# Kernel optimization log

Hardware: AMD Instinct MI355X
Metric: run time of the kernel (lower is better)

## Reference

```python
import jax, jax.numpy as jnp
import numpy as np

B, G, C = 16384, 7, 30  # batch, 7x7 grid, 2*5 box params + 20 classes


def setup_inputs() -> dict:
    key = jax.random.key(0)
    k1, k2 = jax.random.split(key)
    pred = jax.random.uniform(k1, (B, G, G, C), dtype=jnp.float32)
    labels = jax.random.uniform(k2, (B, G, G, C), dtype=jnp.float32)
    # channel 0 of labels is the object-presence indicator (==1 where a gt box exists)
    labels = labels.at[..., 0].set((labels[..., 0] > 0.7).astype(jnp.float32))
    return {"pred": pred, "labels": labels}


def _corners(box):
    # box channels: [conf, x, y, w, h]
    x, y, w, h = box[..., 1], box[..., 2], box[..., 3], box[..., 4]
    return x - 0.5 * w, x + 0.5 * w, y - 0.5 * h, y + 0.5 * h  # left,right,top,bottom


def _iou(b1, b2):
    l1, r1, t1, bt1 = _corners(b1)
    l2, r2, t2, bt2 = _corners(b2)
    in_h = jnp.minimum(bt1, bt2) - jnp.maximum(t1, t2)
    in_w = jnp.minimum(r1, r2) - jnp.maximum(l1, l2)
    inter = jnp.where((in_h < 0) | (in_w < 0), 0.0, in_h * in_w)
    area1 = (bt1 - t1) * (r1 - l1)
    area2 = (bt2 - t2) * (r2 - l2)
    return inter / (area1 + area2 - inter)


def reference(pred, labels):
    mask = labels[..., 0]                     # [B,7,7] object indicator (0/1)
    box1 = pred[..., 0:5]
    box2 = pred[..., 5:10]
    gt = labels[..., 0:5]
    iou1 = _iou(box1, gt)
    iou2 = _iou(box2, gt)
    best = iou1 >= iou2                       # responsible box per cell
    sel = jnp.where(best[..., None], box1, box2)
    iou_max = jnp.where(best, iou1, iou2)
    iou_min = jnp.where(best, iou2, iou1)
    center = 5.0 * ((sel[..., 1] - gt[..., 1]) ** 2 + (sel[..., 2] - gt[..., 2]) ** 2)
    wh = 5.0 * ((jnp.sqrt(sel[..., 3]) - jnp.sqrt(gt[..., 3])) ** 2
                + (jnp.sqrt(sel[..., 4]) - jnp.sqrt(gt[..., 4])) ** 2)
    cls = jnp.sum((pred[..., 10:] - labels[..., 10:]) ** 2, axis=-1)

    def msum(x):
        return jnp.sum(x * mask)

    # [center, wh, obj_conf, noobj_conf, classification]
    return jnp.stack([msum(center), msum(wh), msum(iou_max), msum(iou_min), msum(cls)])
```

## Files before the change

### kernel.cpp

```cpp
#include <hip/hip_runtime.h>
#include <stdint.h>

#define NCH   30
#define TPB   256
#define CPB   256
#define WORDS (CPB * NCH)
#define TOTW  (2 * WORDS)
#define NF4   (TOTW / 4)
#define ITERS (NF4 / TPB)

__device__ __forceinline__ float iou_f(float x1, float y1, float w1, float h1,
                                       float x2, float y2, float w2, float h2) {
    float l1 = x1 - 0.5f * w1, r1 = x1 + 0.5f * w1;
    float t1 = y1 - 0.5f * h1, b1 = y1 + 0.5f * h1;
    float l2 = x2 - 0.5f * w2, r2 = x2 + 0.5f * w2;
    float t2 = y2 - 0.5f * h2, b2 = y2 + 0.5f * h2;
    float in_h = fminf(b1, b2) - fmaxf(t1, t2);
    float in_w = fminf(r1, r2) - fmaxf(l1, l2);
    float inter = (in_h < 0.f || in_w < 0.f) ? 0.f : in_h * in_w;
    float a1 = (b1 - t1) * (r1 - l1);
    float a2 = (b2 - t2) * (r2 - l2);
    return inter / (a1 + a2 - inter);
}

__global__ __launch_bounds__(TPB) void yolo_partial(const float* __restrict__ pred,
                                                    const float* __restrict__ lab,
                                                    float* __restrict__ partial,
                                                    int n_cells) {
    __shared__ float s[TOTW];
    __shared__ float red[5][TPB / 64];

    const int tid = threadIdx.x;
    const int base_cell = blockIdx.x * CPB;
    const size_t base_word = (size_t)base_cell * NCH;
    const int cells_here = min(CPB, n_cells - base_cell);

    if (cells_here == CPB) {
#pragma unroll
        for (int it = 0; it < ITERS; ++it) {
            const int idx = it * TPB + tid;
            const float* src = (idx < WORDS / 4)
                ? (pred + base_word + (size_t)idx * 4)
                : (lab  + base_word + (size_t)(idx - WORDS / 4) * 4);
            __builtin_amdgcn_global_load_lds(
                (const __attribute__((address_space(1))) uint32_t*)src,
                (__attribute__((address_space(3))) uint32_t*)(s + idx * 4),
                16, 0, 0);
        }
    } else {
        const int nw = cells_here * NCH;
        for (int w = tid; w < nw; w += TPB) {
            s[w]         = pred[base_word + w];
            s[WORDS + w] = lab [base_word + w];
        }
    }
    __syncthreads();

    float v0 = 0.f, v1 = 0.f, v2 = 0.f, v3 = 0.f, v4 = 0.f;

    if (tid < cells_here) {
        const float* pp = s + tid * NCH;
        const float* lp = s + WORDS + tid * NCH;

        const float2 l01 = *(const float2*)(lp);
        const float mask = l01.x;

        if (mask != 0.f) {
            const float2 l23 = *(const float2*)(lp + 2);
            const float2 l45 = *(const float2*)(lp + 4);
            const float gx = l01.y, gy = l23.x, gw = l23.y, gh = l45.x;

            const float2 p01 = *(const float2*)(pp);
            const float2 p23 = *(const float2*)(pp + 2);
            const float2 p45 = *(const float2*)(pp + 4);
            const float2 p67 = *(const float2*)(pp + 6);
            const float2 p89 = *(const float2*)(pp + 8);

            const float i1 = iou_f(p01.y, p23.x, p23.y, p45.x, gx, gy, gw, gh);
            const float i2 = iou_f(p67.x, p67.y, p89.x, p89.y, gx, gy, gw, gh);
            const bool best = (i1 >= i2);
            const float sx = best ? p01.y : p67.x;
            const float sy = best ? p23.x : p67.y;
            const float sw = best ? p23.y : p89.x;
            const float sh = best ? p45.x : p89.y;
            const float imax = best ? i1 : i2;
            const float imin = best ? i2 : i1;

            const float center = 5.f * ((sx - gx) * (sx - gx) + (sy - gy) * (sy - gy));
            const float dw = sqrtf(sw) - sqrtf(gw);
            const float dh = sqrtf(sh) - sqrtf(gh);
            const float wh = 5.f * (dw * dw + dh * dh);

            float cls = 0.f;
#pragma unroll
            for (int k = 0; k < 10; ++k) {
                const float2 pd = *(const float2*)(pp + 10 + 2 * k);
                const float2 ld = *(const float2*)(lp + 10 + 2 * k);
                const float dx = pd.x - ld.x;
                const float dy = pd.y - ld.y;
                cls += dx * dx + dy * dy;
            }

            v0 = center * mask;
            v1 = wh * mask;
            v2 = imax * mask;
            v3 = imin * mask;
            v4 = cls * mask;
        }
    }

#pragma unroll
    for (int off = 32; off > 0; off >>= 1) {
        v0 += __shfl_down(v0, off);
        v1 += __shfl_down(v1, off);
        v2 += __shfl_down(v2, off);
        v3 += __shfl_down(v3, off);
        v4 += __shfl_down(v4, off);
    }

    const int wave = tid >> 6;
    const int lane = tid & 63;
    if (lane == 0) {
        red[0][wave] = v0;
        red[1][wave] = v1;
        red[2][wave] = v2;
        red[3][wave] = v3;
        red[4][wave] = v4;
    }
    __syncthreads();

    if (tid < 5) {
        float sacc = 0.f;
#pragma unroll
        for (int w = 0; w < TPB / 64; ++w) sacc += red[tid][w];
        partial[(size_t)blockIdx.x * 5 + tid] = sacc;
    }
}

__global__ __launch_bounds__(256) void final_reduce(const float* __restrict__ partial,
                                                    float* __restrict__ out,
                                                    int n_blocks) {
    __shared__ float red[5][4];
    const int tid = threadIdx.x;
    float v0 = 0.f, v1 = 0.f, v2 = 0.f, v3 = 0.f, v4 = 0.f;
    for (int b = tid; b < n_blocks; b += 256) {
        const float* p = partial + (size_t)b * 5;
        v0 += p[0]; v1 += p[1]; v2 += p[2]; v3 += p[3]; v4 += p[4];
    }
#pragma unroll
    for (int off = 32; off > 0; off >>= 1) {
        v0 += __shfl_down(v0, off);
        v1 += __shfl_down(v1, off);
        v2 += __shfl_down(v2, off);
        v3 += __shfl_down(v3, off);
        v4 += __shfl_down(v4, off);
    }
    const int wave = tid >> 6;
    const int lane = tid & 63;
    if (lane == 0) {
        red[0][wave] = v0;
        red[1][wave] = v1;
        red[2][wave] = v2;
        red[3][wave] = v3;
        red[4][wave] = v4;
    }
    __syncthreads();
    if (tid < 5) {
        float sacc = 0.f;
#pragma unroll
        for (int w = 0; w < 4; ++w) sacc += red[tid][w];
        out[tid] = sacc;
    }
}

extern "C" void kernel_launch(void* const* d_in, const int* in_sizes, int n_in,
                              void* d_out, int out_size, void* d_ws, size_t ws_size,
                              hipStream_t stream) {
    const float* pred = (const float*)d_in[0];
    const float* lab  = (const float*)d_in[1];
    float* out = (float*)d_out;
    float* partial = (float*)d_ws;

    const int n_cells = in_sizes[0] / NCH;
    const int grid = (n_cells + CPB - 1) / CPB;

    hipLaunchKernelGGL(yolo_partial, dim3(grid), dim3(TPB), 0, stream,
                       pred, lab, partial, n_cells);
    hipLaunchKernelGGL(final_reduce, dim3(1), dim3(256), 0, stream,
                       partial, out, grid);
}
```

Baseline: 208.5 us.

## Use persistent single-wave blocks with double-buffered async LDS tile staging

Replaces one-shot 256-thread blocks with a fixed grid of 1280 single-wave persistent blocks that loop over 64-cell tiles. Each block double-buffers tiles in LDS using global_load_lds with explicit vmcnt waits, so the next tile loads while the current one is computed. Block-level barriers and the cross-wave reduction are removed. The vmcnt(15) count is hand-tuned to the number of loads per tile and would break if tile sizes change; fewer waves in flight per CU may limit memory parallelism.

New measurement: 208.3 us. Within noise of the previous version (-0.1%).

```diff
diff --git a/kernel.cpp b/kernel.cpp
--- a/kernel.cpp
+++ b/kernel.cpp
@@ -1,13 +1,13 @@
 #include <hip/hip_runtime.h>
 #include <stdint.h>
 
-#define NCH   30
-#define TPB   256
-#define CPB   256
-#define WORDS (CPB * NCH)
-#define TOTW  (2 * WORDS)
-#define NF4   (TOTW / 4)
-#define ITERS (NF4 / TPB)
+#define NCH    30
+#define TPW    64
+#define TILE   64
+#define TWORDS (TILE * NCH)
+#define TF4    (2 * TWORDS / 4)
+#define LOADS  (TF4 / TPW)
+#define NBLK   1280
 
 __device__ __forceinline__ float iou_f(float x1, float y1, float w1, float h1,
                                        float x2, float y2, float w2, float h2) {
@@ -23,89 +23,119 @@
     return inter / (a1 + a2 - inter);
 }
 
-__global__ __launch_bounds__(TPB) void yolo_partial(const float* __restrict__ pred,
+__device__ __forceinline__ void stage_tile(const float* __restrict__ pred,
+                                           const float* __restrict__ lab,
+                                           float* __restrict__ buf,
+                                           int tile, int lane) {
+    const size_t base = (size_t)tile * TWORDS;
+#pragma unroll
+    for (int i = 0; i < LOADS; ++i) {
+        const int idx = i * TPW + lane;
+        const float* src = (idx < TWORDS / 4)
+            ? (pred + base + (size_t)idx * 4)
+            : (lab  + base + (size_t)(idx - TWORDS / 4) * 4);
+        __builtin_amdgcn_global_load_lds(
+            (const __attribute__((address_space(1))) uint32_t*)src,
+            (__attribute__((address_space(3))) uint32_t*)(buf + idx * 4),
+            16, 0, 0);
+    }
+}
+
+__device__ __forceinline__ void cell_loss(const float* __restrict__ pp,
+                                          const float* __restrict__ lp,
+                                          float& v0, float& v1, float& v2,
+                                          float& v3, float& v4) {
+    const float2 l01 = *(const float2*)(lp);
+    const float mask = l01.x;
+    if (mask == 0.f) return;
+
+    const float2 l23 = *(const float2*)(lp + 2);
+    const float2 l45 = *(const float2*)(lp + 4);
+    const float gx = l01.y, gy = l23.x, gw = l23.y, gh = l45.x;
+
+    const float2 p01 = *(const float2*)(pp);
+    const float2 p23 = *(const float2*)(pp + 2);
+    const float2 p45 = *(const float2*)(pp + 4);
+    const float2 p67 = *(const float2*)(pp + 6);
+    const float2 p89 = *(const float2*)(pp + 8);
+
+    const float i1 = iou_f(p01.y, p23.x, p23.y, p45.x, gx, gy, gw, gh);
+    const float i2 = iou_f(p67.x, p67.y, p89.x, p89.y, gx, gy, gw, gh);
+    const bool best = (i1 >= i2);
+    const float sx = best ? p01.y : p67.x;
+    const float sy = best ? p23.x : p67.y;
+    const float sw = best ? p23.y : p89.x;
+    const float sh = best ? p45.x : p89.y;
+    const float imax = best ? i1 : i2;
+    const float imin = best ? i2 : i1;
+
+    const float center = 5.f * ((sx - gx) * (sx - gx) + (sy - gy) * (sy - gy));
+    const float dw = sqrtf(sw) - sqrtf(gw);
+    const float dh = sqrtf(sh) - sqrtf(gh);
+    const float wh = 5.f * (dw * dw + dh * dh);
+
+    float cls = 0.f;
+#pragma unroll
+    for (int k = 0; k < 10; ++k) {
+        const float2 pd = *(const float2*)(pp + 10 + 2 * k);
+        const float2 ld = *(const float2*)(lp + 10 + 2 * k);
+        const float dx = pd.x - ld.x;
+        const float dy = pd.y - ld.y;
+        cls += dx * dx + dy * dy;
+    }
+
+    v0 += center * mask;
+    v1 += wh * mask;
+    v2 += imax * mask;
+    v3 += imin * mask;
+    v4 += cls * mask;
+}
+
+__global__ __launch_bounds__(TPW) void yolo_partial(const float* __restrict__ pred,
                                                     const float* __restrict__ lab,
                                                     float* __restrict__ partial,
                                                     int n_cells) {
-    __shared__ float s[TOTW];
-    __shared__ float red[5][TPB / 64];
-
-    const int tid = threadIdx.x;
-    const int base_cell = blockIdx.x * CPB;
-    const size_t base_word = (size_t)base_cell * NCH;
-    const int cells_here = min(CPB, n_cells - base_cell);
-
-    if (cells_here == CPB) {
-#pragma unroll
-        for (int it = 0; it < ITERS; ++it) {
-            const int idx = it * TPB + tid;
-            const float* src = (idx < WORDS / 4)
-                ? (pred + base_word + (size_t)idx * 4)
-                : (lab  + base_word + (size_t)(idx - WORDS / 4) * 4);
-            __builtin_amdgcn_global_load_lds(
-                (const __attribute__((address_space(1))) uint32_t*)src,
-                (__attribute__((address_space(3))) uint32_t*)(s + idx * 4),
-                16, 0, 0);
+    __shared__ float s[4 * TWORDS];
+    const int lane = threadIdx.x;
+    const int bid = blockIdx.x;
+    const int NB = gridDim.x;
+    const int nt = n_cells / TILE;
+
+    float v0 = 0.f, v1 = 0.f, v2 = 0.f, v3 = 0.f, v4 = 0.f;
+
+    float* A = s;
+    float* B = s + 2 * TWORDS;
+
+    if (bid < nt) {
+        stage_tile(pred, lab, A, bid, lane);
+        if (bid + NB < nt) stage_tile(pred, lab, B, bid + NB, lane);
+
+        for (int t = bid; t < nt; t += NB) {
+            const bool more  = (t + NB < nt);
+            const bool more2 = (t + 2 * NB < nt);
+            if (more) {
+                asm volatile("s_waitcnt vmcnt(15)" ::: "memory");
+            } else {
+                asm volatile("s_waitcnt vmcnt(0)" ::: "memory");
+            }
+            __builtin_amdgcn_sched_barrier(0);
+
+            cell_loss(A + lane * NCH, A + TWORDS + lane * NCH, v0, v1, v2, v3, v4);
+
+            if (more2) {
+                asm volatile("s_waitcnt lgkmcnt(0)" ::: "memory");
+                __builtin_amdgcn_sched_barrier(0);
+                stage_tile(pred, lab, A, t + 2 * NB, lane);
+            }
+            float* tmp = A; A = B; B = tmp;
         }
-    } else {
-        const int nw = cells_here * NCH;
-        for (int w = tid; w < nw; w += TPB) {
-            s[w]         = pred[base_word + w];
-            s[WORDS + w] = lab [base_word + w];
-        }
-    }
-    __syncthreads();
-
-    float v0 = 0.f, v1 = 0.f, v2 = 0.f, v3 = 0.f, v4 = 0.f;
-
-    if (tid < cells_here) {
-        const float* pp = s + tid * NCH;
-        const float* lp = s + WORDS + tid * NCH;
-
-        const float2 l01 = *(const float2*)(lp);
-        const float mask = l01.x;
-
-        if (mask != 0.f) {
-            const float2 l23 = *(const float2*)(lp + 2);
-            const float2 l45 = *(const float2*)(lp + 4);
-            const float gx = l01.y, gy = l23.x, gw = l23.y, gh = l45.x;
-
-            const float2 p01 = *(const float2*)(pp);
-            const float2 p23 = *(const float2*)(pp + 2);
-            const float2 p45 = *(const float2*)(pp + 4);
-            const float2 p67 = *(const float2*)(pp + 6);
-            const float2 p89 = *(const float2*)(pp + 8);
-
-            const float i1 = iou_f(p01.y, p23.x, p23.y, p45.x, gx, gy, gw, gh);
-            const float i2 = iou_f(p67.x, p67.y, p89.x, p89.y, gx, gy, gw, gh);
-            const bool best = (i1 >= i2);
-            const float sx = best ? p01.y : p67.x;
-            const float sy = best ? p23.x : p67.y;
-            const float sw = best ? p23.y : p89.x;
-            const float sh = best ? p45.x : p89.y;
-            const float imax = best ? i1 : i2;
-            const float imin = best ? i2 : i1;
-
-            const float center = 5.f * ((sx - gx) * (sx - gx) + (sy - gy) * (sy - gy));
-            const float dw = sqrtf(sw) - sqrtf(gw);
-            const float dh = sqrtf(sh) - sqrtf(gh);
-            const float wh = 5.f * (dw * dw + dh * dh);
-
-            float cls = 0.f;
-#pragma unroll
-            for (int k = 0; k < 10; ++k) {
-                const float2 pd = *(const float2*)(pp + 10 + 2 * k);
-                const float2 ld = *(const float2*)(lp + 10 + 2 * k);
-                const float dx = pd.x - ld.x;
-                const float dy = pd.y - ld.y;
-                cls += dx * dx + dy * dy;
-            }
-
-            v0 = center * mask;
-            v1 = wh * mask;
-            v2 = imax * mask;
-            v3 = imin * mask;
-            v4 = cls * mask;
+    }
+
+    const int rem_start = nt * TILE;
+    if (bid == 0 && rem_start < n_cells) {
+        for (int c = rem_start + lane; c < n_cells; c += TPW) {
+            cell_loss(pred + (size_t)c * NCH, lab + (size_t)c * NCH,
+                      v0, v1, v2, v3, v4);
         }
     }
 
@@ -117,23 +147,9 @@
         v3 += __shfl_down(v3, off);
         v4 += __shfl_down(v4, off);
     }
-
-    const int wave = tid >> 6;
-    const int lane = tid & 63;
     if (lane == 0) {
-        red[0][wave] = v0;
-        red[1][wave] = v1;
-        red[2][wave] = v2;
-        red[3][wave] = v3;
-        red[4][wave] = v4;
-    }
-    __syncthreads();
-
-    if (tid < 5) {
-        float sacc = 0.f;
-#pragma unroll
-        for (int w = 0; w < TPB / 64; ++w) sacc += red[tid][w];
-        partial[(size_t)blockIdx.x * 5 + tid] = sacc;
+        float* p = partial + (size_t)bid * 5;
+        p[0] = v0; p[1] = v1; p[2] = v2; p[3] = v3; p[4] = v4;
     }
 }
 
@@ -182,10 +198,9 @@
     float* partial = (float*)d_ws;
 
     const int n_cells = in_sizes[0] / NCH;
-    const int grid = (n_cells + CPB - 1) / CPB;
-
-    hipLaunchKernelGGL(yolo_partial, dim3(grid), dim3(TPB), 0, stream,
+
+    hipLaunchKernelGGL(yolo_partial, dim3(NBLK), dim3(TPW), 0, stream,
                        pred, lab, partial, n_cells);
     hipLaunchKernelGGL(final_reduce, dim3(1), dim3(256), 0, stream,
-                       partial, out, grid);
-}
+                       partial, out, NBLK);
+}
```
